# Optimization experiments

Hardware: AMD Instinct MI355X
Metric: run time of the kernel (lower is better)

Reference implementation:

```python
import jax, jax.numpy as jnp
import numpy as np

R, C, E, H = 64, 2048, 128, 8  # num_rows(cells), num_cols(genes), embed_dim, heads
HD = E // H

def setup_inputs() -> dict:
    key = jax.random.key(0)
    ks = jax.random.split(key, 7)
    s = 1.0 / np.sqrt(E)
    return {
        "x": jax.random.normal(ks[0], (R, C, E), dtype=jnp.float32),
        "Wq": jax.random.normal(ks[1], (E, E), dtype=jnp.float32) * s,
        "bq": jax.random.normal(ks[2], (E,), dtype=jnp.float32) * 0.01,
        "Wk": jax.random.normal(ks[3], (E, E), dtype=jnp.float32) * s,
        "bk": jax.random.normal(ks[4], (E,), dtype=jnp.float32) * 0.01,
        "Wv": jax.random.normal(ks[5], (E, E), dtype=jnp.float32) * s,
        "bv": jax.random.normal(ks[6], (E,), dtype=jnp.float32) * 0.01,
    }

def reference(x, Wq, bq, Wk, bk, Wv, bv):
    num_rows, num_cols, embed_dim = x.shape
    head_dim = embed_dim // H

    def proj(W, b):
        # (R,C,E) -> (R,C,H,hd) -> (H,C,R,hd)
        y = (x @ W.T + b).reshape(num_rows, num_cols, H, head_dim)
        return jnp.transpose(y, (2, 1, 0, 3))

    q = proj(Wq, bq)
    k = proj(Wk, bk)
    v = proj(Wv, bv)

    # softmax over head_dim for q (before flattening rows into features)
    q = jax.nn.softmax(q, axis=-1).reshape(H, num_cols, num_rows * head_dim)
    k = k.reshape(H, num_cols, num_rows * head_dim)
    v = v.reshape(H, num_cols, num_rows * head_dim)

    dim = q.shape[-1]  # num_rows * head_dim
    k = jax.nn.softmax(k, axis=-2)      # softmax over sequence (num_cols)
    q = q * (dim ** -0.5)

    attn_weights = jnp.einsum('hnd,hmd->hnm', q, k)   # (H, C, C)
    context = jnp.einsum('hnd,hne->hde', k, v)        # (H, D, D)
    out = jnp.einsum('hnd,hde->hne', q, context)      # (H, C, D)

    out = out.reshape(H, num_cols, num_rows, head_dim)
    out = jnp.transpose(out, (2, 1, 0, 3)).reshape(num_rows, num_cols, embed_dim)
    return (out, attn_weights)
```

## Files before the change

kernel.cpp:

```cpp
#include <hip/hip_runtime.h>
#include <hip/hip_bf16.h>
#include <stdint.h>

typedef unsigned short u16;
typedef __attribute__((ext_vector_type(8))) short s16x8;
typedef __attribute__((ext_vector_type(4))) float f32x4;

__device__ __forceinline__ u16 f2bf(float f) {
    union { float f; uint32_t u; } v; v.f = f;
    uint32_t r = v.u + 0x7fffu + ((v.u >> 16) & 1u);
    return (u16)(r >> 16);
}
__device__ __forceinline__ float bf2f(u16 b) {
    union { uint32_t u; float f; } v; v.u = ((uint32_t)b) << 16;
    return v.f;
}
__device__ __forceinline__ void split2(float f, u16& h, u16& l) {
    h = f2bf(f);
    l = f2bf(f - bf2f(h));
}

__device__ __forceinline__ void load_lds16(const void* g, void* l) {
    __builtin_amdgcn_global_load_lds(
        (const __attribute__((address_space(1))) unsigned int*)g,
        (__attribute__((address_space(3))) unsigned int*)l,
        16, 0, 0);
}

__global__ __launch_bounds__(256)
void wsplit_kernel(const float* __restrict__ Wq, const float* __restrict__ Wk,
                   const float* __restrict__ Wv, u16* __restrict__ Wsp)
{
    const int i = blockIdx.x * 256 + threadIdx.x;
    const int p  = i >> 14;
    const int r  = i & 16383;
    const int s  = r >> 12;
    const int r2 = r & 4095;
    const int e  = r2 >> 5;
    const int kk = r2 & 31;
    const float* W = (p == 0) ? Wq : (p == 1) ? Wk : Wv;
    const float v = W[e * 128 + s * 32 + kk];
    u16 h, l; split2(v, h, l);
    const size_t base = (size_t)(p * 4 + s) * 10240;
    Wsp[base + e * 40 + kk]        = h;
    Wsp[base + 5120 + e * 40 + kk] = l;
}

__global__ __launch_bounds__(256, 2)
void proj_kernel(const float* __restrict__ x, const u16* __restrict__ Wsp,
                 const float* __restrict__ bq, const float* __restrict__ bk,
                 const float* __restrict__ bv,
                 u16* __restrict__ Qs, float* __restrict__ KTf, u16* __restrict__ VT)
{
    __shared__ __align__(16) u16 Xh[64 * 136], Xl[64 * 136];
    __shared__ __align__(16) u16 Wlds[2][10240];
    const int tid = threadIdx.x;
    const int i0 = blockIdx.x * 64;
    const int r  = i0 >> 11;
    const int c0 = i0 & 2047;

    {
        const char* wsrc = (const char*)Wsp;
        char* wdst = (char*)&Wlds[0][0];
        #pragma unroll
        for (int i = 0; i < 5; ++i)
            load_lds16(wsrc + i * 4096 + tid * 16, wdst + i * 4096 + tid * 16);
    }

    {
        const int col = (tid & 31) * 4;
        const int rb  = tid >> 5;
        #pragma unroll
        for (int pp = 0; pp < 8; ++pp) {
            int row = pp * 8 + rb;
            float4 v = *(const float4*)(x + (size_t)(i0 + row) * 128 + col);
            ushort4 hi, lo;
            split2(v.x, hi.x, lo.x); split2(v.y, hi.y, lo.y);
            split2(v.z, hi.z, lo.z); split2(v.w, hi.w, lo.w);
            *(ushort4*)&Xh[row * 136 + col] = hi;
            *(ushort4*)&Xl[row * 136 + col] = lo;
        }
    }
    __syncthreads();

    const int lane = tid & 63;
    const int w = tid >> 6;
    const int wr = w >> 1, wc = w & 1;
    const int lr = lane & 15, kc = lane >> 4;
    const f32x4 fzero = {0.f, 0.f, 0.f, 0.f};

    const float* const bp[3] = { bq, bk, bv };

    #pragma unroll
    for (int p = 0; p < 3; ++p) {
        f32x4 acc[2][4];
        #pragma unroll
        for (int m = 0; m < 2; ++m)
            #pragma unroll
            for (int n = 0; n < 4; ++n) acc[m][n] = fzero;

        #pragma unroll
        for (int s = 0; s < 4; ++s) {
            const int idx = p * 4 + s;
            if (idx < 11) {
                const char* wsrc = (const char*)Wsp + (size_t)(idx + 1) * 20480;
                char* wdst = (char*)&Wlds[(idx + 1) & 1][0];
                #pragma unroll
                for (int i = 0; i < 5; ++i)
                    load_lds16(wsrc + i * 4096 + tid * 16, wdst + i * 4096 + tid * 16);
            }

            const u16* wbuf = Wlds[idx & 1];
            s16x8 ah[2], al[2];
            #pragma unroll
            for (int m = 0; m < 2; ++m) {
                ah[m] = *(const s16x8*)&Xh[(wr*32 + m*16 + lr) * 136 + s*32 + kc*8];
                al[m] = *(const s16x8*)&Xl[(wr*32 + m*16 + lr) * 136 + s*32 + kc*8];
            }
            #pragma unroll
            for (int n = 0; n < 4; ++n) {
                const u16* wrow = wbuf + (wc*64 + n*16 + lr) * 40 + kc*8;
                s16x8 bh = *(const s16x8*)wrow;
                s16x8 bl = *(const s16x8*)(wrow + 5120);
                #pragma unroll
                for (int m = 0; m < 2; ++m) {
                    acc[m][n] = __builtin_amdgcn_mfma_f32_16x16x32_bf16(ah[m], bh, acc[m][n], 0, 0, 0);
                    acc[m][n] = __builtin_amdgcn_mfma_f32_16x16x32_bf16(al[m], bh, acc[m][n], 0, 0, 0);
                    acc[m][n] = __builtin_amdgcn_mfma_f32_16x16x32_bf16(ah[m], bl, acc[m][n], 0, 0, 0);
                }
            }
            __syncthreads();
        }

        float bvals[4];
        #pragma unroll
        for (int n = 0; n < 4; ++n) bvals[n] = bp[p][wc*64 + n*16 + lr];

        if (p == 0) {
            #pragma unroll
            for (int m = 0; m < 2; ++m) {
                #pragma unroll
                for (int n = 0; n < 4; ++n) {
                    const int h  = wc*4 + n;
                    const int cb = c0 + wr*32 + m*16 + kc*4;
                    #pragma unroll
                    for (int j = 0; j < 4; ++j) {
                        float v = acc[m][n][j] + bvals[n];
                        float mx = v;
                        #pragma unroll
                        for (int s = 8; s >= 1; s >>= 1)
                            mx = fmaxf(mx, __shfl_xor(mx, s, 16));
                        float e = __expf(v - mx);
                        float sm = e;
                        #pragma unroll
                        for (int s = 8; s >= 1; s >>= 1)
                            sm += __shfl_xor(sm, s, 16);
                        float o = e / sm * 0.03125f;
                        Qs[((size_t)h * 2048 + cb + j) * 1024 + r*16 + lr] = f2bf(o);
                    }
                }
            }
        } else if (p == 1) {
            #pragma unroll
            for (int m = 0; m < 2; ++m) {
                #pragma unroll
                for (int n = 0; n < 4; ++n) {
                    const int h  = wc*4 + n;
                    const int cb = c0 + wr*32 + m*16 + kc*4;
                    float4 pk;
                    pk.x = acc[m][n][0] + bvals[n];
                    pk.y = acc[m][n][1] + bvals[n];
                    pk.z = acc[m][n][2] + bvals[n];
                    pk.w = acc[m][n][3] + bvals[n];
                    *(float4*)&KTf[((size_t)(h*1024 + r*16 + lr)) * 2048 + cb] = pk;
                }
            }
        } else {
            #pragma unroll
            for (int m = 0; m < 2; ++m) {
                #pragma unroll
                for (int n = 0; n < 4; ++n) {
                    const int h  = wc*4 + n;
                    const int cb = c0 + wr*32 + m*16 + kc*4;
                    ushort4 pk;
                    pk.x = f2bf(acc[m][n][0] + bvals[n]);
                    pk.y = f2bf(acc[m][n][1] + bvals[n]);
                    pk.z = f2bf(acc[m][n][2] + bvals[n]);
                    pk.w = f2bf(acc[m][n][3] + bvals[n]);
                    *(ushort4*)&VT[((size_t)(h*1024 + r*16 + lr)) * 2048 + cb] = pk;
                }
            }
        }
    }
}

__global__ __launch_bounds__(256)
void ksm_kernel(const float* __restrict__ KTf, u16* __restrict__ KTsm)
{
    const float* p = KTf + (size_t)blockIdx.x * 2048;
    u16* o = KTsm + (size_t)blockIdx.x * 2048;
    const int t = threadIdx.x;
    float4 a = *(const float4*)(p + t * 8);
    float4 b = *(const float4*)(p + t * 8 + 4);
    float v[8] = {a.x, a.y, a.z, a.w, b.x, b.y, b.z, b.w};
    float mx = v[0];
    #pragma unroll
    for (int j = 1; j < 8; ++j) mx = fmaxf(mx, v[j]);
    #pragma unroll
    for (int s = 32; s >= 1; s >>= 1) mx = fmaxf(mx, __shfl_xor(mx, s, 64));
    __shared__ float redm[4], reds[4];
    const int w = t >> 6;
    if ((t & 63) == 0) redm[w] = mx;
    __syncthreads();
    mx = fmaxf(fmaxf(redm[0], redm[1]), fmaxf(redm[2], redm[3]));
    float e[8]; float sm = 0.f;
    #pragma unroll
    for (int j = 0; j < 8; ++j) { e[j] = __expf(v[j] - mx); sm += e[j]; }
    #pragma unroll
    for (int s = 32; s >= 1; s >>= 1) sm += __shfl_xor(sm, s, 64);
    if ((t & 63) == 0) reds[w] = sm;
    __syncthreads();
    sm = reds[0] + reds[1] + reds[2] + reds[3];
    const float inv = 1.f / sm;
    uint4 ov; u16* op = (u16*)&ov;
    #pragma unroll
    for (int j = 0; j < 8; ++j) op[j] = f2bf(e[j] * inv);
    *(uint4*)(o + t * 8) = ov;
}

__global__ __launch_bounds__(256)
void ktrans_kernel(const u16* __restrict__ KTsm, u16* __restrict__ Ksm)
{
    const int h  = blockIdx.z;
    const int d0 = blockIdx.y * 64;
    const int c0 = blockIdx.x * 64;
    __shared__ u16 tile[64][72];
    const int t = threadIdx.x;
    #pragma unroll
    for (int i = 0; i < 2; ++i) {
        int g = t + i * 256;
        int dr = g >> 3;
        int cc = (g & 7) * 8;
        uint4 val = *(const uint4*)(KTsm + ((size_t)(h * 1024 + d0 + dr)) * 2048 + c0 + cc);
        *(uint4*)&tile[dr][cc] = val;
    }
    __syncthreads();
    #pragma unroll
    for (int i = 0; i < 2; ++i) {
        int g = t + i * 256;
        int cr = g >> 3;
        int dc = (g & 7) * 8;
        uint4 ov; u16* op = (u16*)&ov;
        #pragma unroll
        for (int j = 0; j < 8; ++j) op[j] = tile[dc + j][cr];
        *(uint4*)(Ksm + ((size_t)(h * 2048 + c0 + cr)) * 1024 + d0 + dc) = ov;
    }
}

template<int MODE>
__global__ __launch_bounds__(256, 2)
void gemm_bt(const u16* __restrict__ Aall, const u16* __restrict__ Ball,
             float* __restrict__ outF, u16* __restrict__ outB,
             const int M, const int N, const int K)
{
    const int gx = gridDim.x, gy = gridDim.y;
    const int perh = gx * gy;
    int flat = blockIdx.x + gx * (blockIdx.y + gy * blockIdx.z);
    flat = (flat & 7) * perh + (flat >> 3);
    const int h   = flat / perh;
    const int rem = flat - h * perh;
    const int m0  = (rem / gx) * 128;
    const int n0  = (rem % gx) * 128;
    const u16* A = Aall + (size_t)h * M * K;
    const u16* B = Ball + (size_t)h * N * K;
    __shared__ u16 As[128 * 64];
    __shared__ u16 Bs[128 * 64];
    const int tid = threadIdx.x;
    const int lane = tid & 63;
    const int w = tid >> 6;
    const int wr = w >> 1, wc = w & 1;
    const int lr = lane & 15, kc = lane >> 4;
    const f32x4 fzero = {0.f, 0.f, 0.f, 0.f};

    f32x4 acc[4][4];
    #pragma unroll
    for (int m = 0; m < 4; ++m)
        #pragma unroll
        for (int n = 0; n < 4; ++n) acc[m][n] = fzero;

    const int srow = tid >> 3;
    const int scol = (tid & 7) * 8;
    const u16* ga = A + (size_t)(m0 + srow) * K + scol;
    const u16* gb = B + (size_t)(n0 + srow) * K + scol;
    char* lA = (char*)As + tid * 16;
    char* lB = (char*)Bs + tid * 16;
    const size_t rstep = (size_t)32 * K;

    for (int k0 = 0; k0 < K; k0 += 64) {
        __syncthreads();
        load_lds16(ga,             lA);
        load_lds16(ga +     rstep, lA + 4096);
        load_lds16(ga + 2 * rstep, lA + 8192);
        load_lds16(ga + 3 * rstep, lA + 12288);
        load_lds16(gb,             lB);
        load_lds16(gb +     rstep, lB + 4096);
        load_lds16(gb + 2 * rstep, lB + 8192);
        load_lds16(gb + 3 * rstep, lB + 12288);
        ga += 64; gb += 64;
        __syncthreads();

        #pragma unroll
        for (int kk = 0; kk < 64; kk += 32) {
            s16x8 a[4], b[4];
            #pragma unroll
            for (int m = 0; m < 4; ++m)
                a[m] = *(const s16x8*)((const char*)As + (((wr*64 + m*16 + lr) * 64) + kk + kc*8) * 2);
            #pragma unroll
            for (int n = 0; n < 4; ++n)
                b[n] = *(const s16x8*)((const char*)Bs + (((wc*64 + n*16 + lr) * 64) + kk + kc*8) * 2);
            #pragma unroll
            for (int m = 0; m < 4; ++m)
                #pragma unroll
                for (int n = 0; n < 4; ++n)
                    acc[m][n] = __builtin_amdgcn_mfma_f32_16x16x32_bf16(a[m], b[n], acc[m][n], 0, 0, 0);
        }
    }

    #pragma unroll
    for (int m = 0; m < 4; ++m) {
        #pragma unroll
        for (int n = 0; n < 4; ++n) {
            const int grow0 = m0 + wr*64 + m*16 + kc*4;
            const int gcol  = n0 + wc*64 + n*16 + lr;
            #pragma unroll
            for (int j = 0; j < 4; ++j) {
                const float v = acc[m][n][j];
                const int grow = grow0 + j;
                if (MODE == 0) {
                    __builtin_nontemporal_store(v, &outF[(size_t)h * M * N + (size_t)grow * N + gcol]);
                } else if (MODE == 1) {
                    outB[(size_t)h * M * N + (size_t)grow * N + gcol] = f2bf(v);
                } else {
                    const int rr = gcol >> 4, hd = gcol & 15;
                    __builtin_nontemporal_store(v, &outF[((size_t)rr * 2048 + grow) * 128 + h * 16 + hd]);
                }
            }
        }
    }
}

extern "C" void kernel_launch(void* const* d_in, const int* in_sizes, int n_in,
                              void* d_out, int out_size, void* d_ws, size_t ws_size,
                              hipStream_t stream)
{
    const float* x  = (const float*)d_in[0];
    const float* Wq = (const float*)d_in[1];
    const float* bq = (const float*)d_in[2];
    const float* Wk = (const float*)d_in[3];
    const float* bk = (const float*)d_in[4];
    const float* Wv = (const float*)d_in[5];
    const float* bv = (const float*)d_in[6];

    float* outT = (float*)d_out;
    float* attn = outT + (size_t)64 * 2048 * 128;

    u16* Qs   = (u16*)d_ws;
    u16* Ksm  = Qs + (size_t)8 * 2048 * 1024;
    u16* KTsm = (u16*)outT;
    u16*   VT  = (u16*)attn;
    u16*   CT  = VT + (size_t)8 * 1024 * 2048;
    float* KTf = (float*)(CT + (size_t)8 * 1024 * 1024);
    u16*   Wsp = (u16*)(KTf + (size_t)8 * 1024 * 2048);

    wsplit_kernel<<<192, 256, 0, stream>>>(Wq, Wk, Wv, Wsp);
    proj_kernel<<<2048, 256, 0, stream>>>(x, Wsp, bq, bk, bv, Qs, KTf, VT);
    ksm_kernel<<<8192, 256, 0, stream>>>(KTf, KTsm);
    ktrans_kernel<<<dim3(32, 16, 8), 256, 0, stream>>>(KTsm, Ksm);
    gemm_bt<1><<<dim3(8, 8, 8),  256, 0, stream>>>(VT, KTsm, nullptr, CT, 1024, 1024, 2048);
    gemm_bt<2><<<dim3(8, 16, 8), 256, 0, stream>>>(Qs, CT, outT, nullptr, 2048, 1024, 1024);
    gemm_bt<0><<<dim3(16, 16, 8), 256, 0, stream>>>(Qs, Ksm, attn, nullptr, 2048, 2048, 1024);
}
```

Before: 504.5 us.

## Double-buffer LDS tiles in gemm_bt with K-step 32 and higher occupancy

```diff
diff --git a/kernel.cpp b/kernel.cpp
--- a/kernel.cpp
+++ b/kernel.cpp
@@ -258,7 +258,7 @@
 }
 
 template<int MODE>
-__global__ __launch_bounds__(256, 2)
+__global__ __launch_bounds__(256, 4)
 void gemm_bt(const u16* __restrict__ Aall, const u16* __restrict__ Ball,
              float* __restrict__ outF, u16* __restrict__ outB,
              const int M, const int N, const int K)
@@ -273,8 +273,8 @@
     const int n0  = (rem % gx) * 128;
     const u16* A = Aall + (size_t)h * M * K;
     const u16* B = Ball + (size_t)h * N * K;
-    __shared__ u16 As[128 * 64];
-    __shared__ u16 Bs[128 * 64];
+    __shared__ u16 As[2][128 * 32];
+    __shared__ u16 Bs[2][128 * 32];
     const int tid = threadIdx.x;
     const int lane = tid & 63;
     const int w = tid >> 6;
@@ -288,42 +288,46 @@
         #pragma unroll
         for (int n = 0; n < 4; ++n) acc[m][n] = fzero;
 
-    const int srow = tid >> 3;
-    const int scol = (tid & 7) * 8;
+    const int srow = tid >> 2;
+    const int scol = (tid & 3) * 8;
     const u16* ga = A + (size_t)(m0 + srow) * K + scol;
     const u16* gb = B + (size_t)(n0 + srow) * K + scol;
-    char* lA = (char*)As + tid * 16;
-    char* lB = (char*)Bs + tid * 16;
-    const size_t rstep = (size_t)32 * K;
-
-    for (int k0 = 0; k0 < K; k0 += 64) {
+    const size_t rstep = (size_t)64 * K;
+    const int nt = K >> 5;
+
+    auto stage = [&](int buf, int t) {
+        const u16* sa = ga + t * 32;
+        const u16* sb = gb + t * 32;
+        char* lA = (char*)&As[buf][0] + tid * 16;
+        char* lB = (char*)&Bs[buf][0] + tid * 16;
+        load_lds16(sa,         lA);
+        load_lds16(sa + rstep, lA + 4096);
+        load_lds16(sb,         lB);
+        load_lds16(sb + rstep, lB + 4096);
+    };
+
+    stage(0, 0);
+    __syncthreads();
+
+    for (int t = 0; t < nt; ++t) {
+        if (t + 1 < nt) stage((t + 1) & 1, t + 1);
+
+        const u16* as = &As[t & 1][0];
+        const u16* bs = &Bs[t & 1][0];
+        s16x8 a[4], b[4];
+        #pragma unroll
+        for (int m = 0; m < 4; ++m)
+            a[m] = *(const s16x8*)((const char*)as + (((wr*64 + m*16 + lr) * 32) + kc*8) * 2);
+        #pragma unroll
+        for (int n = 0; n < 4; ++n)
+            b[n] = *(const s16x8*)((const char*)bs + (((wc*64 + n*16 + lr) * 32) + kc*8) * 2);
+        #pragma unroll
+        for (int m = 0; m < 4; ++m)
+            #pragma unroll
+            for (int n = 0; n < 4; ++n)
+                acc[m][n] = __builtin_amdgcn_mfma_f32_16x16x32_bf16(a[m], b[n], acc[m][n], 0, 0, 0);
+
         __syncthreads();
-        load_lds16(ga,             lA);
-        load_lds16(ga +     rstep, lA + 4096);
-        load_lds16(ga + 2 * rstep, lA + 8192);
-        load_lds16(ga + 3 * rstep, lA + 12288);
-        load_lds16(gb,             lB);
-        load_lds16(gb +     rstep, lB + 4096);
-        load_lds16(gb + 2 * rstep, lB + 8192);
-        load_lds16(gb + 3 * rstep, lB + 12288);
-        ga += 64; gb += 64;
-        __syncthreads();
-
-        #pragma unroll
-        for (int kk = 0; kk < 64; kk += 32) {
-            s16x8 a[4], b[4];
-            #pragma unroll
-            for (int m = 0; m < 4; ++m)
-                a[m] = *(const s16x8*)((const char*)As + (((wr*64 + m*16 + lr) * 64) + kk + kc*8) * 2);
-            #pragma unroll
-            for (int n = 0; n < 4; ++n)
-                b[n] = *(const s16x8*)((const char*)Bs + (((wc*64 + n*16 + lr) * 64) + kk + kc*8) * 2);
-            #pragma unroll
-            for (int m = 0; m < 4; ++m)
-                #pragma unroll
-                for (int n = 0; n < 4; ++n)
-                    acc[m][n] = __builtin_amdgcn_mfma_f32_16x16x32_bf16(a[m], b[n], acc[m][n], 0, 0, 0);
-        }
     }
 
     #pragma unroll
```

After: 510.5 us. About the same (+1.2%).
